# Optimization experiments

Measured on AMD Instinct MI355X. Metric: run time of the kernel, lower is better.

Reference implementation:

```python
import jax, jax.numpy as jnp
import numpy as np
from jax import lax

B, T, LAT, F2, H = 128, 512, 256, 64, 512
D_IN1 = LAT + F2  # gru5 input dim = 320


def hard_sigmoid(x):
    return jnp.clip(0.2 * x + 0.5, 0.0, 1.0)


def gru_seq(x, W, U, b_in, b_rec, hidden):
    """Keras GRU, reset_after=True, tanh / hard_sigmoid, return_sequences.
    x: [B,T,D], W: [D,3H], U: [H,3H], b_in/b_rec: [3H] -> [B,T,H]."""
    xW = jnp.einsum('btd,dk->btk', x, W) + b_in  # [B,T,3H]
    h0 = jnp.zeros((x.shape[0], hidden), x.dtype)

    def step(h, xt):  # xt: [B,3H]
        inner = h @ U + b_rec
        iz, ir, ih = jnp.split(inner, 3, axis=-1)
        xz, xr, xh = jnp.split(xt, 3, axis=-1)
        zg = hard_sigmoid(xz + iz)
        rg = hard_sigmoid(xr + ir)
        hh = jnp.tanh(xh + rg * ih)
        h_new = zg * h + (1.0 - zg) * hh
        return h_new, h_new

    _, hs = lax.scan(step, h0, jnp.swapaxes(xW, 0, 1))  # [T,B,H]
    return jnp.swapaxes(hs, 0, 1)


def setup_inputs() -> dict:
    key = jax.random.key(0)
    ks = jax.random.split(key, 14)
    s = lambda fan: 1.0 / np.sqrt(fan)
    return {
        'z': jax.random.normal(ks[0], (B, LAT), jnp.float32),
        'train_input_two': jax.random.normal(ks[1], (B, T, F2), jnp.float32),
        'masks': jax.random.uniform(ks[2], (B, T, 1), jnp.float32),
        'dec_masks': jax.random.uniform(ks[3], (B, T, 1), jnp.float32),
        'W5': jax.random.normal(ks[4], (D_IN1, 3 * H), jnp.float32) * s(D_IN1),
        'U5': jax.random.normal(ks[5], (H, 3 * H), jnp.float32) * s(H),
        'bi5': jnp.zeros((3 * H,), jnp.float32),
        'br5': jnp.zeros((3 * H,), jnp.float32),
        'W6': jax.random.normal(ks[6], (H, 3 * H), jnp.float32) * s(H),
        'U6': jax.random.normal(ks[7], (H, 3 * H), jnp.float32) * s(H),
        'bi6': jnp.zeros((3 * H,), jnp.float32),
        'br6': jnp.zeros((3 * H,), jnp.float32),
        'Wd': jax.random.normal(ks[8], (H, 1), jnp.float32) * s(H),
        'bd': jnp.zeros((1,), jnp.float32),
    }


def reference(z, train_input_two, masks, dec_masks,
              W5, U5, bi5, br5, W6, U6, bi6, br6, Wd, bd):
    # RepeatVector: [B,LAT] -> [B,T,LAT]
    rep = jnp.broadcast_to(z[:, None, :], (z.shape[0], T, z.shape[1]))
    concat = jnp.concatenate([rep, train_input_two], axis=-1)  # [B,T,LAT+F2]
    masked = concat * masks                                     # CustomMasking
    g5 = gru_seq(masked, W5, U5, bi5, br5, H)                   # [B,T,H]
    g6 = gru_seq(g5, W6, U6, bi6, br6, H)                       # [B,T,H]
    dec = jnp.tanh(jnp.einsum('bth,ho->bto', g6, Wd) + bd)      # TimeDistributed Dense(1, tanh)
    return dec * dec_masks                                      # [B,T,1]
```

## Files before the change

### kernel.cpp

```cpp
#include <hip/hip_runtime.h>
#include <hip/hip_bf16.h>

typedef unsigned short u16;
typedef unsigned int u32;
typedef unsigned long long u64;
typedef __attribute__((ext_vector_type(8))) short bf16x8;
typedef __attribute__((ext_vector_type(4))) float f32x4;

#define MFMA(a,b,c) __builtin_amdgcn_mfma_f32_16x16x32_bf16((a),(b),(c),0,0,0)
#define AGENT __HIP_MEMORY_SCOPE_AGENT


__device__ __forceinline__ u16 f2bf(float f) {
    u32 u = __float_as_uint(f);
    u32 r = (u + 0x7fffu + ((u >> 16) & 1u)) >> 16;
    return (u16)r;
}
__device__ __forceinline__ float bf2f(u16 v) { return __uint_as_float(((u32)v) << 16); }
__device__ __forceinline__ float sat01(float x) { return fminf(1.f, fmaxf(0.f, x)); }
__device__ __forceinline__ float ftanh(float x) {
    x = fminf(10.f, fmaxf(-10.f, x));
    float e = __expf(2.f * x);
    return (e - 1.f) / (e + 1.f);
}

__device__ __forceinline__ bf16x8 loadB(const float* __restrict__ M, int k0, int colbase,
                                        int l15, int q8) {
    const float* p = M + (size_t)(k0 + q8) * 1536 + colbase + l15;
    bf16x8 r;
#pragma unroll
    for (int j = 0; j < 8; ++j) r[j] = (short)f2bf(p[(size_t)j * 1536]);
    return r;
}

__device__ __forceinline__ bf16x8 ldsA(const u16* s, int stride, int colbase, int l15, int q8) {
    return *(const bf16x8*)(s + l15 * stride + colbase + q8);
}

__global__ void zero_ws_kernel(u32* ws) {
    int i = blockIdx.x * 256 + threadIdx.x;
    if (i < 524544) ws[i] = 0u;
}

__global__ void __launch_bounds__(256, 1)
gru_fused(const float* __restrict__ zin, const float* __restrict__ x2,
          const float* __restrict__ msk, const float* __restrict__ dmsk,
          const float* __restrict__ W5, const float* __restrict__ U5,
          const float* __restrict__ bi5, const float* __restrict__ br5,
          const float* __restrict__ W6, const float* __restrict__ U6,
          const float* __restrict__ bi6, const float* __restrict__ br6,
          const float* __restrict__ Wd, const float* __restrict__ bdp,
          float* __restrict__ out, u32* __restrict__ h5w,
          u32* __restrict__ h6w, u32* __restrict__ cc5)
{
    const int wg = blockIdx.x;
    const int rgp = wg & 7;
    const int q = wg >> 3;
    const bool is6 = q >= 16;
    const int slice = q & 15;
    const int row0 = rgp << 4;
    const int sb = slice << 5;
    const int tid = threadIdx.x;
    const int wv = tid >> 6, lane = tid & 63;
    const int l15 = lane & 15, q8 = (lane >> 4) << 3;

    __shared__ u16 stg[16 * 1032];
    __shared__ float exch[8 * 272];
    __shared__ float mkl[16];

    const int ct = wv & 1;
    const int gMain = (wv < 2) ? 0 : 1;
    const int colMain = gMain * 512 + sb + ct * 16;
    const int colH = 1024 + sb + ct * 16;

    const float* bi = is6 ? bi6 : bi5;
    const float* br = is6 ? br6 : br5;
    const float biasM = bi[colMain + l15] + br[colMain + l15];
    const float biasS = (wv < 2) ? bi[colH + l15] : br[colH + l15];

    float hold0 = 0.f, hold1 = 0.f;
    const int grow = tid >> 4, cp = tid & 15;
    const int c2p = cp >> 3, ccb = (cp & 7) * 2;
    const int r_ = tid >> 4, cth = tid & 15;
    const int b_ = row0 + r_;

    float wdv[8]; float bdv = 0.f;

    if (!is6) {
        bf16x8 Bx[2], Bxs[2], Bh[16], Bhs[16];
#pragma unroll
        for (int kt = 0; kt < 2; ++kt) Bx[kt] = loadB(W5, 256 + kt * 32, colMain, l15, q8);
#pragma unroll
        for (int kt = 0; kt < 16; ++kt) Bh[kt] = loadB(U5, kt * 32, colMain, l15, q8);
        if (wv < 2) {
#pragma unroll
            for (int kt = 0; kt < 2; ++kt) Bxs[kt] = loadB(W5, 256 + kt * 32, colH, l15, q8);
        } else {
#pragma unroll
            for (int kt = 0; kt < 16; ++kt) Bhs[kt] = loadB(U5, kt * 32, colH, l15, q8);
        }

        for (int c = cth; c < 256; c += 16) stg[r_ * 584 + c] = f2bf(zin[b_ * 256 + c]);
        __syncthreads();
        f32x4 zaccM = {0.f, 0.f, 0.f, 0.f}, zaccS = {0.f, 0.f, 0.f, 0.f};
        for (int kt = 0; kt < 8; ++kt) {
            bf16x8 a = ldsA(stg, 584, kt * 32, l15, q8);
            bf16x8 bz = loadB(W5, kt * 32, colMain, l15, q8);
            zaccM = MFMA(a, bz, zaccM);
            if (wv < 2) {
                bf16x8 bz2 = loadB(W5, kt * 32, colH, l15, q8);
                zaccS = MFMA(a, bz2, zaccS);
            }
        }
        __syncthreads();

        for (int t = 0; t < 512; ++t) {
            const u64* src = (const u64*)(h5w + ((t + 3) & 3) * 65536) + (size_t)b_ * 256;
            const u32 exp = (u32)t;
            u64 v[16];
#pragma unroll
            for (int k = 0; k < 16; ++k)
                v[k] = __hip_atomic_load(&src[cth + 16 * k], __ATOMIC_RELAXED, AGENT);
            float mk = msk[b_ * 512 + t];
#pragma unroll
            for (int i = 0; i < 4; ++i) {
                int c = cth + 16 * i;
                stg[r_ * 584 + c] = f2bf(x2[(b_ * 512 + t) * 64 + c] * mk);
            }
            if (tid < 16) mkl[tid] = msk[(row0 + tid) * 512 + t];
            for (;;) {
                bool ok = true;
#pragma unroll
                for (int k = 0; k < 16; ++k) {
                    u32 lo = (u32)v[k], hi = (u32)(v[k] >> 32);
                    if (((lo >> 16) != exp) | ((hi >> 16) != exp)) ok = false;
                }
                if (ok) break;
                __builtin_amdgcn_s_sleep(1);
#pragma unroll
                for (int k = 0; k < 16; ++k)
                    v[k] = __hip_atomic_load(&src[cth + 16 * k], __ATOMIC_RELAXED, AGENT);
            }
#pragma unroll
            for (int k = 0; k < 16; ++k) {
                u32 lo = (u32)v[k], hi = (u32)(v[k] >> 32);
                *(u32*)&stg[r_ * 584 + 64 + 2 * (cth + 16 * k)] = (lo & 0xffffu) | (hi << 16);
            }
            __syncthreads();
            float mkr[4];
#pragma unroll
            for (int i = 0; i < 4; ++i) mkr[i] = mkl[(lane >> 4) * 4 + i];
            f32x4 a0, a1;
#pragma unroll
            for (int i = 0; i < 4; ++i) a0[i] = biasM + mkr[i] * zaccM[i];
            if (wv < 2) {
#pragma unroll
                for (int i = 0; i < 4; ++i) a1[i] = biasS + mkr[i] * zaccS[i];
#pragma unroll
                for (int kt = 0; kt < 2; ++kt) {
                    bf16x8 a = ldsA(stg, 584, kt * 32, l15, q8);
                    a0 = MFMA(a, Bx[kt], a0);
                    a1 = MFMA(a, Bxs[kt], a1);
                }
#pragma unroll
                for (int kt = 0; kt < 16; ++kt) {
                    bf16x8 a = ldsA(stg, 584, 64 + kt * 32, l15, q8);
                    a0 = MFMA(a, Bh[kt], a0);
                }
            } else {
#pragma unroll
                for (int i = 0; i < 4; ++i) a1[i] = biasS;
#pragma unroll
                for (int kt = 0; kt < 2; ++kt) {
                    bf16x8 a = ldsA(stg, 584, kt * 32, l15, q8);
                    a0 = MFMA(a, Bx[kt], a0);
                }
#pragma unroll
                for (int kt = 0; kt < 16; ++kt) {
                    bf16x8 a = ldsA(stg, 584, 64 + kt * 32, l15, q8);
                    a0 = MFMA(a, Bh[kt], a0);
                    a1 = MFMA(a, Bhs[kt], a1);
                }
            }
            {
                int uM = gMain * 2 + ct, uS = (wv < 2 ? 4 + ct : 6 + ct);
#pragma unroll
                for (int i = 0; i < 4; ++i) {
                    int rr = (lane >> 4) * 4 + i;
                    exch[uM * 272 + rr * 17 + l15] = a0[i];
                    exch[uS * 272 + rr * 17 + l15] = a1[i];
                }
            }
            __syncthreads();
            {
                int base0 = (0 + c2p) * 272 + grow * 17 + ccb;
                int base1 = (2 + c2p) * 272 + grow * 17 + ccb;
                int base2 = (4 + c2p) * 272 + grow * 17 + ccb;
                int base3 = (6 + c2p) * 272 + grow * 17 + ccb;
                float zv0 = exch[base0], zv1 = exch[base0 + 1];
                float rv0 = exch[base1], rv1 = exch[base1 + 1];
                float xh0 = exch[base2], xh1 = exch[base2 + 1];
                float ih0 = exch[base3], ih1 = exch[base3 + 1];
                float zg0 = sat01(0.2f * zv0 + 0.5f), zg1 = sat01(0.2f * zv1 + 0.5f);
                float rt0 = sat01(0.2f * rv0 + 0.5f), rt1 = sat01(0.2f * rv1 + 0.5f);
                float hh0 = ftanh(xh0 + rt0 * ih0), hh1 = ftanh(xh1 + rt1 * ih1);
                float h0 = zg0 * hold0 + (1.f - zg0) * hh0;
                float h1 = zg1 * hold1 + (1.f - zg1) * hh1;
                hold0 = h0; hold1 = h1;
                if (t >= 4) {
                    const u32 need = 16u * (u32)(t - 3);
                    while (__hip_atomic_load(&cc5[rgp * 32], __ATOMIC_RELAXED, AGENT) < need)
                        __builtin_amdgcn_s_sleep(1);
                }
                const u32 tg = (u32)(t + 1) << 16;
                u64 w = ((u64)(tg | (u32)f2bf(h1)) << 32) | (u64)(tg | (u32)f2bf(h0));
                u64* dst = (u64*)(h5w + (t & 3) * 65536);
                __hip_atomic_store(&dst[((row0 + grow) * 512 + sb + cp * 2) >> 1], w,
                                   __ATOMIC_RELAXED, AGENT);
            }
        }
    } else {
        bf16x8 Bm[32], Bs[16];
#pragma unroll
        for (int kt = 0; kt < 16; ++kt) Bm[kt] = loadB(W6, kt * 32, colMain, l15, q8);
#pragma unroll
        for (int kt = 0; kt < 16; ++kt) Bm[16 + kt] = loadB(U6, kt * 32, colMain, l15, q8);
        if (wv < 2) {
#pragma unroll
            for (int kt = 0; kt < 16; ++kt) Bs[kt] = loadB(W6, kt * 32, colH, l15, q8);
        } else {
#pragma unroll
            for (int kt = 0; kt < 16; ++kt) Bs[kt] = loadB(U6, kt * 32, colH, l15, q8);
        }
        if (wv == 0) {
#pragma unroll
            for (int j = 0; j < 8; ++j) wdv[j] = Wd[lane * 8 + j];
            bdv = bdp[0];
        }

        for (int t = 1; t <= 513; ++t) {
            const u64* s2 = (const u64*)(h6w + ((t + 2) & 3) * 65536) + (size_t)b_ * 256;
            const u32 exp2 = (u32)(t - 1);
            if (t <= 512) {
                const u64* s1 = (const u64*)(h5w + ((t + 3) & 3) * 65536) + (size_t)b_ * 256;
                const u32 exp1 = (u32)t;
                u64 v1[16], v2[16];
#pragma unroll
                for (int k = 0; k < 16; ++k) {
                    v1[k] = __hip_atomic_load(&s1[cth + 16 * k], __ATOMIC_RELAXED, AGENT);
                    v2[k] = __hip_atomic_load(&s2[cth + 16 * k], __ATOMIC_RELAXED, AGENT);
                }
                for (;;) {
                    bool ok = true;
#pragma unroll
                    for (int k = 0; k < 16; ++k) {
                        u32 lo1 = (u32)v1[k], hi1 = (u32)(v1[k] >> 32);
                        u32 lo2 = (u32)v2[k], hi2 = (u32)(v2[k] >> 32);
                        if (((lo1 >> 16) != exp1) | ((hi1 >> 16) != exp1) |
                            ((lo2 >> 16) != exp2) | ((hi2 >> 16) != exp2)) ok = false;
                    }
                    if (ok) break;
                    __builtin_amdgcn_s_sleep(1);
#pragma unroll
                    for (int k = 0; k < 16; ++k) {
                        v1[k] = __hip_atomic_load(&s1[cth + 16 * k], __ATOMIC_RELAXED, AGENT);
                        v2[k] = __hip_atomic_load(&s2[cth + 16 * k], __ATOMIC_RELAXED, AGENT);
                    }
                }
#pragma unroll
                for (int k = 0; k < 16; ++k) {
                    u32 lo = (u32)v1[k], hi = (u32)(v1[k] >> 32);
                    *(u32*)&stg[r_ * 1032 + 2 * (cth + 16 * k)] = (lo & 0xffffu) | (hi << 16);
                    lo = (u32)v2[k]; hi = (u32)(v2[k] >> 32);
                    *(u32*)&stg[r_ * 1032 + 512 + 2 * (cth + 16 * k)] = (lo & 0xffffu) | (hi << 16);
                }
            } else {
                u64 v2[16];
#pragma unroll
                for (int k = 0; k < 16; ++k)
                    v2[k] = __hip_atomic_load(&s2[cth + 16 * k], __ATOMIC_RELAXED, AGENT);
                for (;;) {
                    bool ok = true;
#pragma unroll
                    for (int k = 0; k < 16; ++k) {
                        u32 lo = (u32)v2[k], hi = (u32)(v2[k] >> 32);
                        if (((lo >> 16) != exp2) | ((hi >> 16) != exp2)) ok = false;
                    }
                    if (ok) break;
                    __builtin_amdgcn_s_sleep(1);
#pragma unroll
                    for (int k = 0; k < 16; ++k)
                        v2[k] = __hip_atomic_load(&s2[cth + 16 * k], __ATOMIC_RELAXED, AGENT);
                }
#pragma unroll
                for (int k = 0; k < 16; ++k) {
                    u32 lo = (u32)v2[k], hi = (u32)(v2[k] >> 32);
                    *(u32*)&stg[r_ * 1032 + 512 + 2 * (cth + 16 * k)] = (lo & 0xffffu) | (hi << 16);
                }
            }
            __syncthreads();
            if (t <= 512 && tid == 0)
                __hip_atomic_fetch_add(&cc5[rgp * 32], 1u, __ATOMIC_RELAXED, AGENT);
            f32x4 a0 = {biasM, biasM, biasM, biasM};
            f32x4 a1 = {biasS, biasS, biasS, biasS};
            if (t <= 512) {
                if (wv < 2) {
#pragma unroll
                    for (int kt = 0; kt < 16; ++kt) {
                        bf16x8 a = ldsA(stg, 1032, kt * 32, l15, q8);
                        a0 = MFMA(a, Bm[kt], a0);
                        a1 = MFMA(a, Bs[kt], a1);
                    }
#pragma unroll
                    for (int kt = 0; kt < 16; ++kt) {
                        bf16x8 a = ldsA(stg, 1032, 512 + kt * 32, l15, q8);
                        a0 = MFMA(a, Bm[16 + kt], a0);
                    }
                } else {
#pragma unroll
                    for (int kt = 0; kt < 16; ++kt) {
                        bf16x8 a = ldsA(stg, 1032, kt * 32, l15, q8);
                        a0 = MFMA(a, Bm[kt], a0);
                    }
#pragma unroll
                    for (int kt = 0; kt < 16; ++kt) {
                        bf16x8 a = ldsA(stg, 1032, 512 + kt * 32, l15, q8);
                        a0 = MFMA(a, Bm[16 + kt], a0);
                        a1 = MFMA(a, Bs[kt], a1);
                    }
                }
            }
            if (t >= 2 && wv == 0) {
                const u16* hrow = &stg[slice * 1032 + 512 + lane * 8];
                bf16x8 hv = *(const bf16x8*)hrow;
                float s = 0.f;
#pragma unroll
                for (int j = 0; j < 8; ++j) s += bf2f((u16)hv[j]) * wdv[j];
#pragma unroll
                for (int off = 32; off >= 1; off >>= 1) s += __shfl_down(s, off);
                if (lane == 0) {
                    int bb = row0 + slice, tt = t - 2;
                    out[bb * 512 + tt] = ftanh(s + bdv) * dmsk[bb * 512 + tt];
                }
            }
            if (t <= 512) {
                {
                    int uM = gMain * 2 + ct, uS = (wv < 2 ? 4 + ct : 6 + ct);
#pragma unroll
                    for (int i = 0; i < 4; ++i) {
                        int rr = (lane >> 4) * 4 + i;
                        exch[uM * 272 + rr * 17 + l15] = a0[i];
                        exch[uS * 272 + rr * 17 + l15] = a1[i];
                    }
                }
                __syncthreads();
                {
                    int base0 = (0 + c2p) * 272 + grow * 17 + ccb;
                    int base1 = (2 + c2p) * 272 + grow * 17 + ccb;
                    int base2 = (4 + c2p) * 272 + grow * 17 + ccb;
                    int base3 = (6 + c2p) * 272 + grow * 17 + ccb;
                    float zv0 = exch[base0], zv1 = exch[base0 + 1];
                    float rv0 = exch[base1], rv1 = exch[base1 + 1];
                    float xh0 = exch[base2], xh1 = exch[base2 + 1];
                    float ih0 = exch[base3], ih1 = exch[base3 + 1];
                    float zg0 = sat01(0.2f * zv0 + 0.5f), zg1 = sat01(0.2f * zv1 + 0.5f);
                    float rt0 = sat01(0.2f * rv0 + 0.5f), rt1 = sat01(0.2f * rv1 + 0.5f);
                    float hh0 = ftanh(xh0 + rt0 * ih0), hh1 = ftanh(xh1 + rt1 * ih1);
                    float h0 = zg0 * hold0 + (1.f - zg0) * hh0;
                    float h1 = zg1 * hold1 + (1.f - zg1) * hh1;
                    hold0 = h0; hold1 = h1;
                    const u32 tg = (u32)t << 16;
                    u64 w = ((u64)(tg | (u32)f2bf(h1)) << 32) | (u64)(tg | (u32)f2bf(h0));
                    u64* dst = (u64*)(h6w + ((t + 3) & 3) * 65536);
                    __hip_atomic_store(&dst[((row0 + grow) * 512 + sb + cp * 2) >> 1], w,
                                       __ATOMIC_RELAXED, AGENT);
                }
            } else {
                __syncthreads();
            }
        }
    }
}

extern "C" void kernel_launch(void* const* d_in, const int* in_sizes, int n_in,
                              void* d_out, int out_size, void* d_ws, size_t ws_size,
                              hipStream_t stream) {
    const float* zin = (const float*)d_in[0];
    const float* x2  = (const float*)d_in[1];
    const float* msk = (const float*)d_in[2];
    const float* dmk = (const float*)d_in[3];
    const float* W5  = (const float*)d_in[4];
    const float* U5  = (const float*)d_in[5];
    const float* bi5 = (const float*)d_in[6];
    const float* br5 = (const float*)d_in[7];
    const float* W6  = (const float*)d_in[8];
    const float* U6  = (const float*)d_in[9];
    const float* bi6 = (const float*)d_in[10];
    const float* br6 = (const float*)d_in[11];
    const float* Wd  = (const float*)d_in[12];
    const float* bd  = (const float*)d_in[13];
    float* out = (float*)d_out;

    u32* h5w = (u32*)d_ws;
    u32* h6w = h5w + 262144;
    u32* cc5 = h6w + 262144;

    zero_ws_kernel<<<dim3(2049), dim3(256), 0, stream>>>((u32*)d_ws);

    gru_fused<<<dim3(256), dim3(256), 0, stream>>>(
        zin, x2, msk, dmk, W5, U5, bi5, br5, W6, U6, bi6, br6,
        Wd, bd, out, h5w, h6w, cc5);
}
```

Measured before the change: 2.577 ms.

## Co-locate both GRU layers in every workgroup with a 16-column slice each

Each workgroup, rather than being assigned to a single GRU layer, now holds a 16-column slice of both layers. Waves 0-1 handle layer 5 and waves 2-3 handle layer 6 in one combined wavefront-pipelined time loop. This removes the cross-workgroup cc5 counter that throttled layer 5 against layer 6, and it halves the per-workgroup column width. The polling now waits on both h5 and h6 buffers in every block. Each wave holds up to 48 bf16x8 weight fragments, which raises register pressure, and the gate update now writes one element per thread as a 32-bit tagged store.

```diff
diff --git a/kernel.cpp b/kernel.cpp
--- a/kernel.cpp
+++ b/kernel.cpp
@@ -33,13 +33,17 @@
     return r;
 }
 
-__device__ __forceinline__ bf16x8 ldsA(const u16* s, int stride, int colbase, int l15, int q8) {
-    return *(const bf16x8*)(s + l15 * stride + colbase + q8);
+#define ST 1096
+#define H5OFF 64
+#define H6OFF 576
+
+__device__ __forceinline__ bf16x8 ldsA(const u16* s, int off, int l15, int q8) {
+    return *(const bf16x8*)(s + l15 * ST + off + q8);
 }
 
 __global__ void zero_ws_kernel(u32* ws) {
     int i = blockIdx.x * 256 + threadIdx.x;
-    if (i < 524544) ws[i] = 0u;
+    if (i < 524288) ws[i] = 0u;
 }
 
 __global__ void __launch_bounds__(256, 1)
@@ -51,333 +55,260 @@
           const float* __restrict__ bi6, const float* __restrict__ br6,
           const float* __restrict__ Wd, const float* __restrict__ bdp,
           float* __restrict__ out, u32* __restrict__ h5w,
-          u32* __restrict__ h6w, u32* __restrict__ cc5)
+          u32* __restrict__ h6w)
 {
     const int wg = blockIdx.x;
     const int rgp = wg & 7;
-    const int q = wg >> 3;
-    const bool is6 = q >= 16;
-    const int slice = q & 15;
+    const int sl = wg >> 3;
     const int row0 = rgp << 4;
-    const int sb = slice << 5;
+    const int sb = sl << 4;
     const int tid = threadIdx.x;
     const int wv = tid >> 6, lane = tid & 63;
     const int l15 = lane & 15, q8 = (lane >> 4) << 3;
 
-    __shared__ u16 stg[16 * 1032];
+    __shared__ u16 stg[16 * ST];
     __shared__ float exch[8 * 272];
     __shared__ float mkl[16];
 
-    const int ct = wv & 1;
-    const int gMain = (wv < 2) ? 0 : 1;
-    const int colMain = gMain * 512 + sb + ct * 16;
-    const int colH = 1024 + sb + ct * 16;
-
-    const float* bi = is6 ? bi6 : bi5;
-    const float* br = is6 ? br6 : br5;
-    const float biasM = bi[colMain + l15] + br[colMain + l15];
-    const float biasS = (wv < 2) ? bi[colH + l15] : br[colH + l15];
-
-    float hold0 = 0.f, hold1 = 0.f;
-    const int grow = tid >> 4, cp = tid & 15;
-    const int c2p = cp >> 3, ccb = (cp & 7) * 2;
+    const int gsel = wv & 1;
+    const bool lay6 = wv >= 2;
+    const int colM = gsel * 512 + sb;
+    const int colS = 1024 + sb;
+    const float* bi = lay6 ? bi6 : bi5;
+    const float* br = lay6 ? br6 : br5;
+    const float biasM = bi[colM + l15] + br[colM + l15];
+    const float biasS = (gsel == 0) ? bi[colS + l15] : br[colS + l15];
+
+    bf16x8 Ba[16], Bb[16], Bc[16];
+    if (wv == 0) {
+#pragma unroll
+        for (int kt = 0; kt < 2; ++kt)  Ba[kt] = loadB(W5, 256 + kt * 32, sb, l15, q8);
+#pragma unroll
+        for (int kt = 0; kt < 16; ++kt) Bb[kt] = loadB(U5, kt * 32, sb, l15, q8);
+#pragma unroll
+        for (int kt = 0; kt < 2; ++kt)  Bc[kt] = loadB(W5, 256 + kt * 32, 1024 + sb, l15, q8);
+    } else if (wv == 1) {
+#pragma unroll
+        for (int kt = 0; kt < 2; ++kt)  Ba[kt] = loadB(W5, 256 + kt * 32, 512 + sb, l15, q8);
+#pragma unroll
+        for (int kt = 0; kt < 16; ++kt) Bb[kt] = loadB(U5, kt * 32, 512 + sb, l15, q8);
+#pragma unroll
+        for (int kt = 0; kt < 16; ++kt) Bc[kt] = loadB(U5, kt * 32, 1024 + sb, l15, q8);
+    } else if (wv == 2) {
+#pragma unroll
+        for (int kt = 0; kt < 16; ++kt) Ba[kt] = loadB(W6, kt * 32, sb, l15, q8);
+#pragma unroll
+        for (int kt = 0; kt < 16; ++kt) Bb[kt] = loadB(U6, kt * 32, sb, l15, q8);
+#pragma unroll
+        for (int kt = 0; kt < 16; ++kt) Bc[kt] = loadB(W6, kt * 32, 1024 + sb, l15, q8);
+    } else {
+#pragma unroll
+        for (int kt = 0; kt < 16; ++kt) Ba[kt] = loadB(W6, kt * 32, 512 + sb, l15, q8);
+#pragma unroll
+        for (int kt = 0; kt < 16; ++kt) Bb[kt] = loadB(U6, kt * 32, 512 + sb, l15, q8);
+#pragma unroll
+        for (int kt = 0; kt < 16; ++kt) Bc[kt] = loadB(U6, kt * 32, 1024 + sb, l15, q8);
+    }
+
+    float wdv[8]; float bdv = bdp[0];
+    if (sl < 16 && wv == 0) {
+#pragma unroll
+        for (int j = 0; j < 8; ++j) wdv[j] = Wd[lane * 8 + j];
+    }
+
     const int r_ = tid >> 4, cth = tid & 15;
     const int b_ = row0 + r_;
 
-    float wdv[8]; float bdv = 0.f;
-
-    if (!is6) {
-        bf16x8 Bx[2], Bxs[2], Bh[16], Bhs[16];
-#pragma unroll
-        for (int kt = 0; kt < 2; ++kt) Bx[kt] = loadB(W5, 256 + kt * 32, colMain, l15, q8);
-#pragma unroll
-        for (int kt = 0; kt < 16; ++kt) Bh[kt] = loadB(U5, kt * 32, colMain, l15, q8);
-        if (wv < 2) {
-#pragma unroll
-            for (int kt = 0; kt < 2; ++kt) Bxs[kt] = loadB(W5, 256 + kt * 32, colH, l15, q8);
-        } else {
-#pragma unroll
-            for (int kt = 0; kt < 16; ++kt) Bhs[kt] = loadB(U5, kt * 32, colH, l15, q8);
-        }
-
-        for (int c = cth; c < 256; c += 16) stg[r_ * 584 + c] = f2bf(zin[b_ * 256 + c]);
-        __syncthreads();
-        f32x4 zaccM = {0.f, 0.f, 0.f, 0.f}, zaccS = {0.f, 0.f, 0.f, 0.f};
+    for (int c = cth; c < 256; c += 16) stg[r_ * ST + H5OFF + c] = f2bf(zin[b_ * 256 + c]);
+    __syncthreads();
+    f32x4 zaccM = {0.f, 0.f, 0.f, 0.f}, zaccS = {0.f, 0.f, 0.f, 0.f};
+    if (wv < 2) {
         for (int kt = 0; kt < 8; ++kt) {
-            bf16x8 a = ldsA(stg, 584, kt * 32, l15, q8);
-            bf16x8 bz = loadB(W5, kt * 32, colMain, l15, q8);
-            zaccM = MFMA(a, bz, zaccM);
-            if (wv < 2) {
-                bf16x8 bz2 = loadB(W5, kt * 32, colH, l15, q8);
-                zaccS = MFMA(a, bz2, zaccS);
-            }
-        }
-        __syncthreads();
-
-        for (int t = 0; t < 512; ++t) {
-            const u64* src = (const u64*)(h5w + ((t + 3) & 3) * 65536) + (size_t)b_ * 256;
-            const u32 exp = (u32)t;
-            u64 v[16];
+            bf16x8 a = ldsA(stg, H5OFF + kt * 32, l15, q8);
+            zaccM = MFMA(a, loadB(W5, kt * 32, colM, l15, q8), zaccM);
+            if (wv == 0)
+                zaccS = MFMA(a, loadB(W5, kt * 32, 1024 + sb, l15, q8), zaccS);
+        }
+    }
+    __syncthreads();
+
+    float hold5 = 0.f, hold6 = 0.f;
+
+    for (int t = 0; t < 514; ++t) {
+        u64 v[16];
+        if (t >= 1) {
+            const u64* s2 = (const u64*)(h6w + ((t + 2) & 3) * 65536) + (size_t)b_ * 256;
+            const u32 exp2 = (u32)(t - 1);
 #pragma unroll
             for (int k = 0; k < 16; ++k)
-                v[k] = __hip_atomic_load(&src[cth + 16 * k], __ATOMIC_RELAXED, AGENT);
-            float mk = msk[b_ * 512 + t];
-#pragma unroll
-            for (int i = 0; i < 4; ++i) {
-                int c = cth + 16 * i;
-                stg[r_ * 584 + c] = f2bf(x2[(b_ * 512 + t) * 64 + c] * mk);
-            }
-            if (tid < 16) mkl[tid] = msk[(row0 + tid) * 512 + t];
+                v[k] = __hip_atomic_load(&s2[cth + 16 * k], __ATOMIC_RELAXED, AGENT);
             for (;;) {
                 bool ok = true;
 #pragma unroll
                 for (int k = 0; k < 16; ++k) {
                     u32 lo = (u32)v[k], hi = (u32)(v[k] >> 32);
-                    if (((lo >> 16) != exp) | ((hi >> 16) != exp)) ok = false;
+                    if (((lo >> 16) != exp2) | ((hi >> 16) != exp2)) ok = false;
                 }
                 if (ok) break;
                 __builtin_amdgcn_s_sleep(1);
 #pragma unroll
                 for (int k = 0; k < 16; ++k)
-                    v[k] = __hip_atomic_load(&src[cth + 16 * k], __ATOMIC_RELAXED, AGENT);
+                    v[k] = __hip_atomic_load(&s2[cth + 16 * k], __ATOMIC_RELAXED, AGENT);
             }
 #pragma unroll
             for (int k = 0; k < 16; ++k) {
                 u32 lo = (u32)v[k], hi = (u32)(v[k] >> 32);
-                *(u32*)&stg[r_ * 584 + 64 + 2 * (cth + 16 * k)] = (lo & 0xffffu) | (hi << 16);
-            }
-            __syncthreads();
+                *(u32*)&stg[r_ * ST + H6OFF + 2 * (cth + 16 * k)] = (lo & 0xffffu) | (hi << 16);
+            }
+        }
+        if (t <= 512) {
+            const u64* s1 = (const u64*)(h5w + ((t + 3) & 3) * 65536) + (size_t)b_ * 256;
+            const u32 exp1 = (u32)t;
+#pragma unroll
+            for (int k = 0; k < 16; ++k)
+                v[k] = __hip_atomic_load(&s1[cth + 16 * k], __ATOMIC_RELAXED, AGENT);
+            if (t < 512) {
+                float mk = msk[b_ * 512 + t];
+#pragma unroll
+                for (int i = 0; i < 4; ++i) {
+                    int c = cth + 16 * i;
+                    stg[r_ * ST + c] = f2bf(x2[(b_ * 512 + t) * 64 + c] * mk);
+                }
+                if (tid < 16) mkl[tid] = msk[(row0 + tid) * 512 + t];
+            }
+            for (;;) {
+                bool ok = true;
+#pragma unroll
+                for (int k = 0; k < 16; ++k) {
+                    u32 lo = (u32)v[k], hi = (u32)(v[k] >> 32);
+                    if (((lo >> 16) != exp1) | ((hi >> 16) != exp1)) ok = false;
+                }
+                if (ok) break;
+                __builtin_amdgcn_s_sleep(1);
+#pragma unroll
+                for (int k = 0; k < 16; ++k)
+                    v[k] = __hip_atomic_load(&s1[cth + 16 * k], __ATOMIC_RELAXED, AGENT);
+            }
+#pragma unroll
+            for (int k = 0; k < 16; ++k) {
+                u32 lo = (u32)v[k], hi = (u32)(v[k] >> 32);
+                *(u32*)&stg[r_ * ST + H5OFF + 2 * (cth + 16 * k)] = (lo & 0xffffu) | (hi << 16);
+            }
+        }
+        __syncthreads();
+
+        const bool do5 = (t < 512);
+        const bool do6 = (t >= 1 && t <= 512);
+        f32x4 a0, a1;
+        if (!lay6 && do5) {
             float mkr[4];
 #pragma unroll
             for (int i = 0; i < 4; ++i) mkr[i] = mkl[(lane >> 4) * 4 + i];
-            f32x4 a0, a1;
 #pragma unroll
             for (int i = 0; i < 4; ++i) a0[i] = biasM + mkr[i] * zaccM[i];
-            if (wv < 2) {
+            if (wv == 0) {
 #pragma unroll
                 for (int i = 0; i < 4; ++i) a1[i] = biasS + mkr[i] * zaccS[i];
 #pragma unroll
                 for (int kt = 0; kt < 2; ++kt) {
-                    bf16x8 a = ldsA(stg, 584, kt * 32, l15, q8);
-                    a0 = MFMA(a, Bx[kt], a0);
-                    a1 = MFMA(a, Bxs[kt], a1);
-                }
+                    bf16x8 a = ldsA(stg, kt * 32, l15, q8);
+                    a0 = MFMA(a, Ba[kt], a0);
+                    a1 = MFMA(a, Bc[kt], a1);
+                }
+#pragma unroll
+                for (int kt = 0; kt < 16; ++kt)
+                    a0 = MFMA(ldsA(stg, H5OFF + kt * 32, l15, q8), Bb[kt], a0);
+            } else {
+#pragma unroll
+                for (int i = 0; i < 4; ++i) a1[i] = biasS;
+#pragma unroll
+                for (int kt = 0; kt < 2; ++kt)
+                    a0 = MFMA(ldsA(stg, kt * 32, l15, q8), Ba[kt], a0);
 #pragma unroll
                 for (int kt = 0; kt < 16; ++kt) {
-                    bf16x8 a = ldsA(stg, 584, 64 + kt * 32, l15, q8);
-                    a0 = MFMA(a, Bh[kt], a0);
-                }
+                    bf16x8 a = ldsA(stg, H5OFF + kt * 32, l15, q8);
+                    a0 = MFMA(a, Bb[kt], a0);
+                    a1 = MFMA(a, Bc[kt], a1);
+                }
+            }
+        }
+        if (lay6 && do6) {
+#pragma unroll
+            for (int i = 0; i < 4; ++i) { a0[i] = biasM; a1[i] = biasS; }
+            if (wv == 2) {
+#pragma unroll
+                for (int kt = 0; kt < 16; ++kt) {
+                    bf16x8 a = ldsA(stg, H5OFF + kt * 32, l15, q8);
+                    a0 = MFMA(a, Ba[kt], a0);
+                    a1 = MFMA(a, Bc[kt], a1);
+                }
+#pragma unroll
+                for (int kt = 0; kt < 16; ++kt)
+                    a0 = MFMA(ldsA(stg, H6OFF + kt * 32, l15, q8), Bb[kt], a0);
             } else {
 #pragma unroll
-                for (int i = 0; i < 4; ++i) a1[i] = biasS;
-#pragma unroll
-                for (int kt = 0; kt < 2; ++kt) {
-                    bf16x8 a = ldsA(stg, 584, kt * 32, l15, q8);
-                    a0 = MFMA(a, Bx[kt], a0);
-                }
+                for (int kt = 0; kt < 16; ++kt)
+                    a0 = MFMA(ldsA(stg, H5OFF + kt * 32, l15, q8), Ba[kt], a0);
 #pragma unroll
                 for (int kt = 0; kt < 16; ++kt) {
-                    bf16x8 a = ldsA(stg, 584, 64 + kt * 32, l15, q8);
-                    a0 = MFMA(a, Bh[kt], a0);
-                    a1 = MFMA(a, Bhs[kt], a1);
-                }
-            }
-            {
-                int uM = gMain * 2 + ct, uS = (wv < 2 ? 4 + ct : 6 + ct);
-#pragma unroll
-                for (int i = 0; i < 4; ++i) {
-                    int rr = (lane >> 4) * 4 + i;
-                    exch[uM * 272 + rr * 17 + l15] = a0[i];
-                    exch[uS * 272 + rr * 17 + l15] = a1[i];
-                }
-            }
-            __syncthreads();
-            {
-                int base0 = (0 + c2p) * 272 + grow * 17 + ccb;
-                int base1 = (2 + c2p) * 272 + grow * 17 + ccb;
-                int base2 = (4 + c2p) * 272 + grow * 17 + ccb;
-                int base3 = (6 + c2p) * 272 + grow * 17 + ccb;
-                float zv0 = exch[base0], zv1 = exch[base0 + 1];
-                float rv0 = exch[base1], rv1 = exch[base1 + 1];
-                float xh0 = exch[base2], xh1 = exch[base2 + 1];
-                float ih0 = exch[base3], ih1 = exch[base3 + 1];
-                float zg0 = sat01(0.2f * zv0 + 0.5f), zg1 = sat01(0.2f * zv1 + 0.5f);
-                float rt0 = sat01(0.2f * rv0 + 0.5f), rt1 = sat01(0.2f * rv1 + 0.5f);
-                float hh0 = ftanh(xh0 + rt0 * ih0), hh1 = ftanh(xh1 + rt1 * ih1);
-                float h0 = zg0 * hold0 + (1.f - zg0) * hh0;
-                float h1 = zg1 * hold1 + (1.f - zg1) * hh1;
-                hold0 = h0; hold1 = h1;
-                if (t >= 4) {
-                    const u32 need = 16u * (u32)(t - 3);
-                    while (__hip_atomic_load(&cc5[rgp * 32], __ATOMIC_RELAXED, AGENT) < need)
-                        __builtin_amdgcn_s_sleep(1);
-                }
-                const u32 tg = (u32)(t + 1) << 16;
-                u64 w = ((u64)(tg | (u32)f2bf(h1)) << 32) | (u64)(tg | (u32)f2bf(h0));
-                u64* dst = (u64*)(h5w + (t & 3) * 65536);
-                __hip_atomic_store(&dst[((row0 + grow) * 512 + sb + cp * 2) >> 1], w,
-                                   __ATOMIC_RELAXED, AGENT);
-            }
-        }
-    } else {
-        bf16x8 Bm[32], Bs[16];
-#pragma unroll
-        for (int kt = 0; kt < 16; ++kt) Bm[kt] = loadB(W6, kt * 32, colMain, l15, q8);
-#pragma unroll
-        for (int kt = 0; kt < 16; ++kt) Bm[16 + kt] = loadB(U6, kt * 32, colMain, l15, q8);
-        if (wv < 2) {
-#pragma unroll
-            for (int kt = 0; kt < 16; ++kt) Bs[kt] = loadB(W6, kt * 32, colH, l15, q8);
-        } else {
-#pragma unroll
-            for (int kt = 0; kt < 16; ++kt) Bs[kt] = loadB(U6, kt * 32, colH, l15, q8);
-        }
-        if (wv == 0) {
-#pragma unroll
-            for (int j = 0; j < 8; ++j) wdv[j] = Wd[lane * 8 + j];
-            bdv = bdp[0];
-        }
-
-        for (int t = 1; t <= 513; ++t) {
-            const u64* s2 = (const u64*)(h6w + ((t + 2) & 3) * 65536) + (size_t)b_ * 256;
-            const u32 exp2 = (u32)(t - 1);
-            if (t <= 512) {
-                const u64* s1 = (const u64*)(h5w + ((t + 3) & 3) * 65536) + (size_t)b_ * 256;
-                const u32 exp1 = (u32)t;
-                u64 v1[16], v2[16];
-#pragma unroll
-                for (int k = 0; k < 16; ++k) {
-                    v1[k] = __hip_atomic_load(&s1[cth + 16 * k], __ATOMIC_RELAXED, AGENT);
-                    v2[k] = __hip_atomic_load(&s2[cth + 16 * k], __ATOMIC_RELAXED, AGENT);
-                }
-                for (;;) {
-                    bool ok = true;
-#pragma unroll
-                    for (int k = 0; k < 16; ++k) {
-                        u32 lo1 = (u32)v1[k], hi1 = (u32)(v1[k] >> 32);
-                        u32 lo2 = (u32)v2[k], hi2 = (u32)(v2[k] >> 32);
-                        if (((lo1 >> 16) != exp1) | ((hi1 >> 16) != exp1) |
-                            ((lo2 >> 16) != exp2) | ((hi2 >> 16) != exp2)) ok = false;
-                    }
-                    if (ok) break;
-                    __builtin_amdgcn_s_sleep(1);
-#pragma unroll
-                    for (int k = 0; k < 16; ++k) {
-                        v1[k] = __hip_atomic_load(&s1[cth + 16 * k], __ATOMIC_RELAXED, AGENT);
-                        v2[k] = __hip_atomic_load(&s2[cth + 16 * k], __ATOMIC_RELAXED, AGENT);
-                    }
-                }
-#pragma unroll
-                for (int k = 0; k < 16; ++k) {
-                    u32 lo = (u32)v1[k], hi = (u32)(v1[k] >> 32);
-                    *(u32*)&stg[r_ * 1032 + 2 * (cth + 16 * k)] = (lo & 0xffffu) | (hi << 16);
-                    lo = (u32)v2[k]; hi = (u32)(v2[k] >> 32);
-                    *(u32*)&stg[r_ * 1032 + 512 + 2 * (cth + 16 * k)] = (lo & 0xffffu) | (hi << 16);
-                }
-            } else {
-                u64 v2[16];
-#pragma unroll
-                for (int k = 0; k < 16; ++k)
-                    v2[k] = __hip_atomic_load(&s2[cth + 16 * k], __ATOMIC_RELAXED, AGENT);
-                for (;;) {
-                    bool ok = true;
-#pragma unroll
-                    for (int k = 0; k < 16; ++k) {
-                        u32 lo = (u32)v2[k], hi = (u32)(v2[k] >> 32);
-                        if (((lo >> 16) != exp2) | ((hi >> 16) != exp2)) ok = false;
-                    }
-                    if (ok) break;
-                    __builtin_amdgcn_s_sleep(1);
-#pragma unroll
-                    for (int k = 0; k < 16; ++k)
-                        v2[k] = __hip_atomic_load(&s2[cth + 16 * k], __ATOMIC_RELAXED, AGENT);
-                }
-#pragma unroll
-                for (int k = 0; k < 16; ++k) {
-                    u32 lo = (u32)v2[k], hi = (u32)(v2[k] >> 32);
-                    *(u32*)&stg[r_ * 1032 + 512 + 2 * (cth + 16 * k)] = (lo & 0xffffu) | (hi << 16);
-                }
-            }
-            __syncthreads();
-            if (t <= 512 && tid == 0)
-                __hip_atomic_fetch_add(&cc5[rgp * 32], 1u, __ATOMIC_RELAXED, AGENT);
-            f32x4 a0 = {biasM, biasM, biasM, biasM};
-            f32x4 a1 = {biasS, biasS, biasS, biasS};
-            if (t <= 512) {
-                if (wv < 2) {
-#pragma unroll
-                    for (int kt = 0; kt < 16; ++kt) {
-                        bf16x8 a = ldsA(stg, 1032, kt * 32, l15, q8);
-                        a0 = MFMA(a, Bm[kt], a0);
-                        a1 = MFMA(a, Bs[kt], a1);
-                    }
-#pragma unroll
-                    for (int kt = 0; kt < 16; ++kt) {
-                        bf16x8 a = ldsA(stg, 1032, 512 + kt * 32, l15, q8);
-                        a0 = MFMA(a, Bm[16 + kt], a0);
-                    }
-                } else {
-#pragma unroll
-                    for (int kt = 0; kt < 16; ++kt) {
-                        bf16x8 a = ldsA(stg, 1032, kt * 32, l15, q8);
-                        a0 = MFMA(a, Bm[kt], a0);
-                    }
-#pragma unroll
-                    for (int kt = 0; kt < 16; ++kt) {
-                        bf16x8 a = ldsA(stg, 1032, 512 + kt * 32, l15, q8);
-                        a0 = MFMA(a, Bm[16 + kt], a0);
-                        a1 = MFMA(a, Bs[kt], a1);
-                    }
-                }
-            }
-            if (t >= 2 && wv == 0) {
-                const u16* hrow = &stg[slice * 1032 + 512 + lane * 8];
-                bf16x8 hv = *(const bf16x8*)hrow;
-                float s = 0.f;
-#pragma unroll
-                for (int j = 0; j < 8; ++j) s += bf2f((u16)hv[j]) * wdv[j];
-#pragma unroll
-                for (int off = 32; off >= 1; off >>= 1) s += __shfl_down(s, off);
-                if (lane == 0) {
-                    int bb = row0 + slice, tt = t - 2;
-                    out[bb * 512 + tt] = ftanh(s + bdv) * dmsk[bb * 512 + tt];
-                }
-            }
-            if (t <= 512) {
-                {
-                    int uM = gMain * 2 + ct, uS = (wv < 2 ? 4 + ct : 6 + ct);
-#pragma unroll
-                    for (int i = 0; i < 4; ++i) {
-                        int rr = (lane >> 4) * 4 + i;
-                        exch[uM * 272 + rr * 17 + l15] = a0[i];
-                        exch[uS * 272 + rr * 17 + l15] = a1[i];
-                    }
-                }
-                __syncthreads();
-                {
-                    int base0 = (0 + c2p) * 272 + grow * 17 + ccb;
-                    int base1 = (2 + c2p) * 272 + grow * 17 + ccb;
-                    int base2 = (4 + c2p) * 272 + grow * 17 + ccb;
-                    int base3 = (6 + c2p) * 272 + grow * 17 + ccb;
-                    float zv0 = exch[base0], zv1 = exch[base0 + 1];
-                    float rv0 = exch[base1], rv1 = exch[base1 + 1];
-                    float xh0 = exch[base2], xh1 = exch[base2 + 1];
-                    float ih0 = exch[base3], ih1 = exch[base3 + 1];
-                    float zg0 = sat01(0.2f * zv0 + 0.5f), zg1 = sat01(0.2f * zv1 + 0.5f);
-                    float rt0 = sat01(0.2f * rv0 + 0.5f), rt1 = sat01(0.2f * rv1 + 0.5f);
-                    float hh0 = ftanh(xh0 + rt0 * ih0), hh1 = ftanh(xh1 + rt1 * ih1);
-                    float h0 = zg0 * hold0 + (1.f - zg0) * hh0;
-                    float h1 = zg1 * hold1 + (1.f - zg1) * hh1;
-                    hold0 = h0; hold1 = h1;
-                    const u32 tg = (u32)t << 16;
-                    u64 w = ((u64)(tg | (u32)f2bf(h1)) << 32) | (u64)(tg | (u32)f2bf(h0));
-                    u64* dst = (u64*)(h6w + ((t + 3) & 3) * 65536);
-                    __hip_atomic_store(&dst[((row0 + grow) * 512 + sb + cp * 2) >> 1], w,
-                                       __ATOMIC_RELAXED, AGENT);
-                }
-            } else {
-                __syncthreads();
-            }
+                    bf16x8 a = ldsA(stg, H6OFF + kt * 32, l15, q8);
+                    a0 = MFMA(a, Bb[kt], a0);
+                    a1 = MFMA(a, Bc[kt], a1);
+                }
+            }
+        }
+        if ((!lay6 && do5) || (lay6 && do6)) {
+            int uM = (lay6 ? 4 : 0) + gsel;
+            int uS = (lay6 ? 6 : 2) + gsel;
+#pragma unroll
+            for (int i = 0; i < 4; ++i) {
+                int rr = (lane >> 4) * 4 + i;
+                exch[uM * 272 + rr * 17 + l15] = a0[i];
+                exch[uS * 272 + rr * 17 + l15] = a1[i];
+            }
+        }
+        if (t >= 2 && wv == 0 && sl < 16) {
+            const u16* hrow = &stg[sl * ST + H6OFF + lane * 8];
+            bf16x8 hv = *(const bf16x8*)hrow;
+            float s = 0.f;
+#pragma unroll
+            for (int j = 0; j < 8; ++j) s += bf2f((u16)hv[j]) * wdv[j];
+#pragma unroll
+            for (int off = 32; off >= 1; off >>= 1) s += __shfl_down(s, off);
+            if (lane == 0) {
+                int tt = t - 2;
+                out[(row0 + sl) * 512 + tt] = ftanh(s + bdv) * dmsk[(row0 + sl) * 512 + tt];
+            }
+        }
+        __syncthreads();
+
+        if (do5) {
+            float zv = exch[0 * 272 + r_ * 17 + cth];
+            float rv = exch[1 * 272 + r_ * 17 + cth];
+            float xh = exch[2 * 272 + r_ * 17 + cth];
+            float ih = exch[3 * 272 + r_ * 17 + cth];
+            float zg = sat01(0.2f * zv + 0.5f);
+            float rg = sat01(0.2f * rv + 0.5f);
+            float hh = ftanh(xh + rg * ih);
+            float hn = zg * hold5 + (1.f - zg) * hh;
+            hold5 = hn;
+            u32 w = ((u32)(t + 1) << 16) | (u32)f2bf(hn);
+            __hip_atomic_store(&h5w[(t & 3) * 65536 + b_ * 512 + sb + cth], w,
+                               __ATOMIC_RELAXED, AGENT);
+        }
+        if (do6) {
+            float zv = exch[4 * 272 + r_ * 17 + cth];
+            float rv = exch[5 * 272 + r_ * 17 + cth];
+            float xh = exch[6 * 272 + r_ * 17 + cth];
+            float ih = exch[7 * 272 + r_ * 17 + cth];
+            float zg = sat01(0.2f * zv + 0.5f);
+            float rg = sat01(0.2f * rv + 0.5f);
+            float hh = ftanh(xh + rg * ih);
+            float hn = zg * hold6 + (1.f - zg) * hh;
+            hold6 = hn;
+            u32 w = ((u32)t << 16) | (u32)f2bf(hn);
+            __hip_atomic_store(&h6w[((t + 3) & 3) * 65536 + b_ * 512 + sb + cth], w,
+                               __ATOMIC_RELAXED, AGENT);
         }
     }
 }
@@ -403,11 +334,10 @@
 
     u32* h5w = (u32*)d_ws;
     u32* h6w = h5w + 262144;
-    u32* cc5 = h6w + 262144;
-
-    zero_ws_kernel<<<dim3(2049), dim3(256), 0, stream>>>((u32*)d_ws);
+
+    zero_ws_kernel<<<dim3(2048), dim3(256), 0, stream>>>((u32*)d_ws);
 
     gru_fused<<<dim3(256), dim3(256), 0, stream>>>(
         zin, x2, msk, dmk, W5, U5, bi5, br5, W6, U6, bi6, br6,
-        Wd, bd, out, h5w, h6w, cc5);
-}
+        Wd, bd, out, h5w, h6w);
+}
```

Result: slower. 2.841 ms (+10.2%).
